# Optimization experiments

Measured on AMD Instinct MI355X. Metric: run time of the kernel, lower is better.

Reference implementation:

```python
import jax, jax.numpy as jnp
import numpy as np

B, H, W, C = 8, 32, 32, 512
NUM_HEADS = 8
NUM_GROUPS = 32
EPS = 1e-5
SKIP_SCALE = 1.0
HEAD_DIM = C // NUM_HEADS


def setup_inputs() -> dict:
    key = jax.random.key(0)
    ks = jax.random.split(key, 7)
    fan_in, fan_out = C, 3 * C
    lim_qkv = np.sqrt(6.0 / (fan_in + fan_out))
    lim_out = 1e-5 * np.sqrt(6.0 / (C + C))
    return {
        "x": jax.random.normal(ks[0], (B, H, W, C), jnp.float32),
        "norm_scale": jnp.ones((C,), jnp.float32),
        "norm_bias": jnp.zeros((C,), jnp.float32),
        "qkv_kernel": jax.random.uniform(ks[1], (C, NUM_HEADS, 3 * HEAD_DIM), jnp.float32, -lim_qkv, lim_qkv),
        "qkv_bias": jnp.zeros((NUM_HEADS, 3 * HEAD_DIM), jnp.float32),
        "out_kernel": jax.random.uniform(ks[2], (NUM_HEADS, HEAD_DIM, C), jnp.float32, -lim_out, lim_out),
        "out_bias": jnp.zeros((C,), jnp.float32),
    }


def group_norm(x, scale, bias):
    # x: (B, S, C); normalize per-group over (S, C//G), flax GroupNorm semantics
    b, s, c = x.shape
    g = NUM_GROUPS
    xg = x.reshape(b, s, g, c // g)
    mean = jnp.mean(xg, axis=(1, 3), keepdims=True)
    var = jnp.var(xg, axis=(1, 3), keepdims=True)
    xg = (xg - mean) * jax.lax.rsqrt(var + EPS)
    return xg.reshape(b, s, c) * scale + bias


def reference(x, norm_scale, norm_bias, qkv_kernel, qkv_bias, out_kernel, out_bias):
    batch_dims = x.shape[:-3]
    h, w, c = x.shape[-3:]
    xi = x.reshape(-1, h * w, c)  # (B, S, C)
    out = group_norm(xi, norm_scale, norm_bias)
    # QKV projection: (B,S,C) x (C, NH, 3*HD) -> (B,S,NH,3*HD)
    qkv = jnp.einsum('bsc,chd->bshd', out, qkv_kernel) + qkv_bias
    q, k, v = jnp.split(qkv, 3, axis=-1)  # each (B,S,NH,HD)
    scale = 1.0 / jnp.sqrt(jnp.sqrt(jnp.asarray(HEAD_DIM, jnp.float32)))
    q = q * scale
    k = k * scale
    attn = jnp.einsum('bqhd,bkhd->bhqk', q, k)
    attn = jax.nn.softmax(attn, axis=-1)
    o = jnp.einsum('bhqk,bkhd->bqhd', attn, v)
    o = jnp.einsum('bqhd,hdc->bqc', o, out_kernel) + out_bias
    o = (o + xi) * SKIP_SCALE
    return o.reshape((*batch_dims, h, w, c))
```

## Files before the change

kernel.cpp:

```cpp
#include <hip/hip_runtime.h>
#include <stdint.h>

typedef __attribute__((ext_vector_type(8))) short short8;
typedef __attribute__((ext_vector_type(4))) float f32x4;
typedef __attribute__((ext_vector_type(16))) float f32x16;
typedef __attribute__((ext_vector_type(4))) unsigned int u32x4;
typedef unsigned short u16;
typedef unsigned int u32;

#define NBATCH 8
#define SLEN 1024
#define CDIM 512
#define NHEADS 8
#define HDIM 64
#define MROWS (NBATCH*SLEN)
#define NQKV (NHEADS*3*HDIM)
#define QK_SCALE 0.35355339059327373f

__device__ inline u16 f2bf(float f){
  union{float f; uint32_t i;} v; v.f=f;
  uint32_t r = v.i + 0x7fffu + ((v.i>>16)&1u);
  return (u16)(r>>16);
}

__device__ inline u32 pk2(float a, float b){
  u32 r;
  asm("v_cvt_pk_bf16_f32 %0, %1, %2" : "=v"(r) : "v"(a), "v"(b));
  return r;
}

__device__ __forceinline__ void gld16(const u16* g, u16* l){
  __builtin_amdgcn_global_load_lds(
    (const __attribute__((address_space(1))) void*)g,
    (__attribute__((address_space(3))) void*)l, 16, 0, 0);
}

template<int N>
__global__ __launch_bounds__(256) void prep_w(const float* __restrict__ w, u16* __restrict__ wt){
  int tk = blockIdx.x / (N/64), tn = blockIdx.x % (N/64);
  int k0 = tk*64, n0 = tn*64;
  int t = threadIdx.x;
  __shared__ u16 lt[64][72];
  int row = t >> 2, slot = t & 3;
  const float* src = w + (size_t)(k0+row)*N + n0 + slot*16;
  #pragma unroll
  for (int j=0;j<16;++j)
    lt[row][slot*16+j] = f2bf(src[j]);
  __syncthreads();
  u16 tmp[16];
  #pragma unroll
  for (int j=0;j<16;++j) tmp[j] = lt[slot*16+j][row];
  *(u32x4*)(wt + (size_t)(n0+row)*512 + k0 + slot*16)     = *(u32x4*)tmp;
  *(u32x4*)(wt + (size_t)(n0+row)*512 + k0 + slot*16 + 8) = *(u32x4*)(tmp+8);
}

__global__ __launch_bounds__(256) void gn_stats(const float* __restrict__ x, float* __restrict__ stats){
  int bid = blockIdx.x;
  int b = bid >> 5, g = bid & 31;
  int t = threadIdx.x;
  const float* base = x + (size_t)b*SLEN*CDIM + g*16;
  float s1=0.f, s2=0.f;
  for (int s = t; s < SLEN; s += 256){
    const float4* p = (const float4*)(base + (size_t)s*CDIM);
    #pragma unroll
    for (int j=0;j<4;++j){
      float4 v = p[j];
      s1 += v.x+v.y+v.z+v.w;
      s2 += v.x*v.x + v.y*v.y + v.z*v.z + v.w*v.w;
    }
  }
  #pragma unroll
  for (int m=1;m<64;m<<=1){ s1 += __shfl_xor(s1,m); s2 += __shfl_xor(s2,m); }
  __shared__ float red[8];
  int wid = t>>6;
  if ((t&63)==0){ red[wid*2]=s1; red[wid*2+1]=s2; }
  __syncthreads();
  if (t==0){
    float a=0,c=0;
    #pragma unroll
    for (int w2=0;w2<4;++w2){ a+=red[w2*2]; c+=red[w2*2+1]; }
    float mean = a*(1.f/16384.f);
    float var  = c*(1.f/16384.f) - mean*mean;
    stats[bid*2]   = mean;
    stats[bid*2+1] = rsqrtf(var + 1e-5f);
  }
}

__global__ __launch_bounds__(256) void norm_cast(const float* __restrict__ x, const float* __restrict__ stats,
                        const float* __restrict__ scale, const float* __restrict__ bias,
                        u16* __restrict__ xn){
  int idx = blockIdx.x*256 + threadIdx.x;
  int m = idx >> 5, g = idx & 31;
  int b = m >> 10;
  float mean = stats[(b*32+g)*2];
  float rstd = stats[(b*32+g)*2+1];
  const float* xp = x + (size_t)m*CDIM + g*16;
  const float* sp = scale + g*16;
  const float* bp = bias + g*16;
  short8 o0, o1;
  #pragma unroll
  for (int j=0;j<16;++j){
    float v = (xp[j]-mean)*rstd*sp[j] + bp[j];
    if (j<8) o0[j] = (short)f2bf(v); else o1[j-8] = (short)f2bf(v);
  }
  short8* dst = (short8*)(xn + (size_t)m*CDIM + g*16);
  dst[0]=o0; dst[1]=o1;
}

#define BM 128
#define BN 128
#define BK 64

template<int EPI, int NT>
__global__ __launch_bounds__(256, 3) void gemm_bf16(
    const u16* __restrict__ A, const u16* __restrict__ Bt,
    const float* __restrict__ bias, const float* __restrict__ resid,
    float* __restrict__ outF,
    u16* __restrict__ qb, u16* __restrict__ kb, u16* __restrict__ vtb)
{
  const int K = CDIM;
  int t = threadIdx.x;
  int l = t & 63, wid = t >> 6;
  int g = l >> 4, c = l & 15;
  int wr = wid >> 1, wc = wid & 1;
  int nwg = gridDim.x;
  int cpx = nwg >> 3;
  int orig = blockIdx.x;
  int swz = (orig & 7)*cpx + (orig >> 3);
  int m0 = (swz / NT) * BM, n0 = (swz % NT) * BN;

  __shared__ __attribute__((aligned(16))) u16 ls[16384];
  char* lsAc = (char*)ls; char* lsBc = (char*)(ls + 8192);

  f32x4 acc[4][4];
  #pragma unroll
  for (int i=0;i<4;++i)
    #pragma unroll
    for(int j=0;j<4;++j) acc[i][j] = (f32x4)0.f;

  int lrow = l >> 3, slot = l & 7;
  int scol = ((slot ^ lrow) << 3);
  const int KT = K / BK;
  for (int kt=0; kt<KT; ++kt){
    __syncthreads();
    int kbo = kt*BK;
    #pragma unroll
    for (int q2=0; q2<4; ++q2){
      int row = wid*32 + q2*8 + lrow;
      gld16(A  + (size_t)(m0+row)*K + kbo + scol, ls        + (wid*4+q2)*512);
      gld16(Bt + (size_t)(n0+row)*K + kbo + scol, ls + 8192 + (wid*4+q2)*512);
    }
    asm volatile("s_waitcnt vmcnt(0)" ::: "memory");
    __syncthreads();
    #pragma unroll
    for (int kk=0; kk<2; ++kk){
      short8 af[4], bfr[4];
      #pragma unroll
      for (int i=0;i<4;++i){
        int rowA = wr*64 + i*16 + c;
        af[i]  = *(const short8*)(lsAc + rowA*128 + ((kk*4+g) ^ (rowA&7))*16);
        int rowB = wc*64 + i*16 + c;
        bfr[i] = *(const short8*)(lsBc + rowB*128 + ((kk*4+g) ^ (rowB&7))*16);
      }
      #pragma unroll
      for (int i=0;i<4;++i)
        #pragma unroll
        for (int j=0;j<4;++j)
          acc[i][j] = __builtin_amdgcn_mfma_f32_16x16x32_bf16(af[i], bfr[j], acc[i][j], 0,0,0);
    }
  }

  if (EPI == 0){
    int b = m0 >> 10, s0 = m0 & (SLEN-1);
    __syncthreads();
    u16* lsC = ls;
    #pragma unroll
    for (int i=0;i<4;++i){
      int rl0 = wr*64 + i*16 + g*4;
      #pragma unroll
      for (int j=0;j<4;++j){
        int cl = wc*64 + j*16 + c;
        int gcol = n0 + cl;
        int jj = gcol % 192;
        float sc_ = (jj < 128) ? QK_SCALE : 1.0f;
        float bv = bias[gcol];
        #pragma unroll
        for (int r=0;r<4;++r)
          lsC[(rl0+r)*128 + cl] = f2bf((acc[i][j][r] + bv)*sc_);
      }
    }
    __syncthreads();
    #pragma unroll
    for (int cc=0; cc<8; ++cc){
      int ch = cc*256 + t;
      int rl = ch >> 4, slot2 = ch & 15;
      int cl = slot2*8;
      int gcol = n0 + cl;
      int h = gcol / 192, jj = gcol % 192;
      int s = s0 + rl;
      u32x4 vv = *(const u32x4*)(lsC + rl*128 + cl);
      size_t rowb = ((size_t)(b*NHEADS+h))*SLEN + s;
      if (jj < 64)       __builtin_nontemporal_store(vv, (u32x4*)(qb + rowb*HDIM + jj));
      else if (jj < 128) __builtin_nontemporal_store(vv, (u32x4*)(kb + rowb*HDIM + (jj-64)));
    }
    int blk3 = (n0 >> 7) % 3;
    if (blk3 != 0){
      __syncthreads();
      u16* lsV = ls;
      #pragma unroll
      for (int i=0;i<4;++i){
        int rl0 = wr*64 + i*16 + g*4;
        #pragma unroll
        for (int j=0;j<4;++j){
          int cl = wc*64 + j*16 + c;
          int jj = (n0 + cl) % 192;
          if (jj >= 128){
            #pragma unroll
            for (int r=0;r<4;++r)
              lsV[(jj-128)*136 + rl0 + r] = f2bf(acc[i][j][r] + bias[n0+cl]);
          }
        }
      }
      __syncthreads();
      int hv = (n0 + ((blk3==1)?0:64)) / 192;
      size_t vbase = ((size_t)(b*NHEADS+hv))*HDIM*SLEN;
      #pragma unroll
      for (int cc=0; cc<4; ++cc){
        int chunk = cc*256 + t;
        int d = chunk >> 4, so = (chunk & 15)*8;
        u32x4 vv = *(const u32x4*)(lsV + d*136 + so);
        __builtin_nontemporal_store(vv, (u32x4*)(vtb + vbase + (size_t)d*SLEN + s0 + so));
      }
    }
  } else {
    #pragma unroll
    for (int i=0;i<4;++i){
      int grow = m0 + wr*64 + i*16 + g*4;
      #pragma unroll
      for (int j=0;j<4;++j){
        int gcol = n0 + wc*64 + j*16 + c;
        float bv = bias[gcol];
        #pragma unroll
        for (int r=0;r<4;++r){
          size_t off = (size_t)(grow+r)*CDIM + gcol;
          float rv = __builtin_nontemporal_load(&resid[off]);
          __builtin_nontemporal_store(acc[i][j][r] + bv + rv, &outF[off]);
        }
      }
    }
  }
}

#define PV_KS(PT, QOFF, KS) { \
    u32 A0 = pk2(PT[QOFF+0], PT[QOFF+1]); \
    u32 A1 = pk2(PT[QOFF+2], PT[QOFF+3]); \
    u32 B0 = pk2(PT[QOFF+4], PT[QOFF+5]); \
    u32 B1 = pk2(PT[QOFF+6], PT[QOFF+7]); \
    u32 A0s = __shfl_xor(A0,32), A1s = __shfl_xor(A1,32); \
    u32 B0s = __shfl_xor(B0,32), B1s = __shfl_xor(B1,32); \
    uint4 w; \
    w.x = hi ? B0s : A0;  w.y = hi ? B1s : A1; \
    w.z = hi ? B0  : A0s; w.w = hi ? B1  : A1s; \
    short8 fP; __builtin_memcpy(&fP, &w, 16); \
    o0 = __builtin_amdgcn_mfma_f32_32x32x16_bf16(fV0[KS], fP, o0, 0,0,0); \
    o1 = __builtin_amdgcn_mfma_f32_32x32x16_bf16(fV1[KS], fP, o1, 0,0,0); }

__global__ __launch_bounds__(256, 2) void attn_fused(const u16* __restrict__ qg,
  const u16* __restrict__ kg, const u16* __restrict__ vtg, u16* __restrict__ og)
{
  int bid = blockIdx.x;
  int nid = (bid & 7)*64 + (bid >> 3);
  int bh = nid >> 3, qi = nid & 7;
  int t = threadIdx.x, l = t & 63, wid = t >> 6;
  int q = l & 31, hi = l >> 5;
  int q0 = qi*128 + wid*32;

  __shared__ __attribute__((aligned(16))) u16 kl[4][4096];
  __shared__ __attribute__((aligned(16))) u16 vl[4][4096];

  const u16* qrow = qg + ((size_t)bh*SLEN + q0 + q)*HDIM + hi*8;
  short8 fQ[4];
  #pragma unroll
  for (int ds=0; ds<4; ++ds) fQ[ds] = *(const short8*)(qrow + ds*16);

  f32x16 o0, o1;
  #pragma unroll
  for (int r=0;r<16;++r){ o0[r]=0.f; o1[r]=0.f; }
  float mr = -1e30f, lsum = 0.f;

  const u16* kt_base = kg  + (size_t)bh*SLEN*HDIM;
  const u16* vt_base = vtg + (size_t)bh*HDIM*SLEN;
  int srow = l >> 3, sslot = l & 7;
  int scol8 = ((sslot ^ srow) << 3);

#define STAGE(BUF, KV) { \
    _Pragma("unroll") \
    for (int j=0;j<2;++j){ \
      int row = wid*16 + j*8 + srow; \
      int chunk = wid*2 + j; \
      gld16(kt_base + (size_t)((KV)*64 + row)*HDIM + scol8, &kl[BUF][chunk*512]); \
      gld16(vt_base + (size_t)row*SLEN + (KV)*64 + scol8,   &vl[BUF][chunk*512]); \
    } }

  STAGE(0, 0)
  STAGE(1, 1)

  int sl_q = q & 7;
  for (int kv=0; kv<16; ++kv){
    int cur = kv & 3;
    if (kv < 14) STAGE((kv+2)&3, kv+2)
    if (kv < 14)      asm volatile("s_waitcnt vmcnt(8)" ::: "memory");
    else if (kv==14)  asm volatile("s_waitcnt vmcnt(4)" ::: "memory");
    else              asm volatile("s_waitcnt vmcnt(0)" ::: "memory");
    __syncthreads();
    const u16* kb_ = &kl[cur][0];
    const u16* vb_ = &vl[cur][0];
    short8 fK0[4], fK1[4];
    #pragma unroll
    for (int ds=0; ds<4; ++ds){
      int sl = ((ds*2+hi) ^ sl_q) << 3;
      fK0[ds] = *(const short8*)(kb_ + q*64 + sl);
      fK1[ds] = *(const short8*)(kb_ + (q+32)*64 + sl);
    }
    f32x16 p0, p1;
    #pragma unroll
    for (int r=0;r<16;++r){ p0[r]=0.f; p1[r]=0.f; }
    __builtin_amdgcn_s_setprio(1);
    #pragma unroll
    for (int ds=0; ds<4; ++ds){
      p0 = __builtin_amdgcn_mfma_f32_32x32x16_bf16(fK0[ds], fQ[ds], p0, 0,0,0);
      p1 = __builtin_amdgcn_mfma_f32_32x32x16_bf16(fK1[ds], fQ[ds], p1, 0,0,0);
    }
    __builtin_amdgcn_s_setprio(0);
    float a8[8];
    #pragma unroll
    for (int r=0;r<8;++r)
      a8[r] = fmaxf(fmaxf(p0[r],p0[r+8]), fmaxf(p1[r],p1[r+8]));
    #pragma unroll
    for (int s=4;s>0;s>>=1)
      #pragma unroll
      for (int r=0;r<4;++r) if (r<s) a8[r] = fmaxf(a8[r], a8[r+s]);
    float tmax = fmaxf(a8[0], __shfl_xor(a8[0], 32));
    if (!__all(tmax <= mr + 8.0f)){
      float mn = fmaxf(mr, tmax);
      float alpha = __expf(mr - mn);
      mr = mn;
      lsum *= alpha;
      #pragma unroll
      for (int r=0;r<16;++r){ o0[r]*=alpha; o1[r]*=alpha; }
    }
    #pragma unroll
    for (int r=0;r<16;++r){ p0[r] = __expf(p0[r]-mr); p1[r] = __expf(p1[r]-mr); }
    short8 fV0[4], fV1[4];
    #pragma unroll
    for (int ks=0; ks<4; ++ks){
      int sl = ((ks*2+hi) ^ sl_q) << 3;
      fV0[ks] = *(const short8*)(vb_ + q*64 + sl);
      fV1[ks] = *(const short8*)(vb_ + (q+32)*64 + sl);
    }
    float s8[8];
    #pragma unroll
    for (int r=0;r<8;++r) s8[r] = (p0[r]+p0[r+8]) + (p1[r]+p1[r+8]);
    #pragma unroll
    for (int s=4;s>0;s>>=1)
      #pragma unroll
      for (int r=0;r<4;++r) if (r<s) s8[r] += s8[r+s];
    float rs = s8[0] + __shfl_xor(s8[0], 32);
    lsum += rs;
    __builtin_amdgcn_s_setprio(1);
    PV_KS(p0, 0, 0)
    PV_KS(p0, 8, 1)
    PV_KS(p1, 0, 2)
    PV_KS(p1, 8, 3)
    __builtin_amdgcn_s_setprio(0);
  }

  float inv = 1.f / lsum;
  int b = bh >> 3, h = bh & 7;
  u16* obase = og + ((size_t)b*SLEN + q0 + q)*CDIM + h*HDIM;
  #pragma unroll
  for (int pr=0; pr<8; ++pr){
    int d = ((2*pr)&3) + 8*(pr>>1) + 4*hi;
    *(u32*)(obase + d)      = pk2(o0[2*pr]*inv, o0[2*pr+1]*inv);
    *(u32*)(obase + 32 + d) = pk2(o1[2*pr]*inv, o1[2*pr+1]*inv);
  }
}

extern "C" void kernel_launch(void* const* d_in, const int* in_sizes, int n_in,
                              void* d_out, int out_size, void* d_ws, size_t ws_size,
                              hipStream_t stream){
  const float* x      = (const float*)d_in[0];
  const float* nscale = (const float*)d_in[1];
  const float* nbias  = (const float*)d_in[2];
  const float* wqkv   = (const float*)d_in[3];
  const float* bqkv   = (const float*)d_in[4];
  const float* wout   = (const float*)d_in[5];
  const float* bout   = (const float*)d_in[6];
  float* out = (float*)d_out;

  char* ws = (char*)d_ws;
  size_t off = 0;
  auto alloc = [&](size_t bytes){ void* p = ws + off; off += (bytes + 255) & ~255ull; return p; };
  float* stats  = (float*)alloc(256*2*sizeof(float));
  u16* wqkv_t = (u16*)alloc((size_t)NQKV*CDIM*2);
  u16* wout_t = (u16*)alloc((size_t)CDIM*CDIM*2);
  u16* xn     = (u16*)alloc((size_t)MROWS*CDIM*2);
  u16* qb     = (u16*)alloc((size_t)MROWS*CDIM*2);
  u16* kb     = (u16*)alloc((size_t)MROWS*CDIM*2);
  u16* vtb    = (u16*)alloc((size_t)MROWS*CDIM*2);
  u16* ob     = (u16*)alloc((size_t)MROWS*CDIM*2);

  prep_w<NQKV><<<dim3(8*(NQKV/64)), dim3(256), 0, stream>>>(wqkv, wqkv_t);
  prep_w<CDIM><<<dim3(8*(CDIM/64)), dim3(256), 0, stream>>>(wout, wout_t);
  gn_stats <<<dim3(256), dim3(256), 0, stream>>>(x, stats);
  norm_cast<<<dim3((MROWS*32)/256), dim3(256), 0, stream>>>(x, stats, nscale, nbias, xn);
  gemm_bf16<0,12><<<dim3(768), dim3(256), 0, stream>>>(xn, wqkv_t, bqkv, nullptr, nullptr, qb, kb, vtb);
  attn_fused<<<dim3(512), dim3(256), 0, stream>>>(qb, kb, vtb, ob);
  gemm_bf16<1,4><<<dim3(256), dim3(256), 0, stream>>>(ob, wout_t, bout, x, out, nullptr, nullptr, nullptr);
}
```

Before: 101.0 us.

## Process two KV tiles per iteration in attention and use permlane32 swaps

After: 95.19 us. -5.7%, faster.

```diff
diff --git a/kernel.cpp b/kernel.cpp
--- a/kernel.cpp
+++ b/kernel.cpp
@@ -251,19 +251,18 @@
   }
 }
 
-#define PV_KS(PT, QOFF, KS) { \
+#define PV_KS(PT, QOFF, V0, V1, KS) { \
     u32 A0 = pk2(PT[QOFF+0], PT[QOFF+1]); \
     u32 A1 = pk2(PT[QOFF+2], PT[QOFF+3]); \
     u32 B0 = pk2(PT[QOFF+4], PT[QOFF+5]); \
     u32 B1 = pk2(PT[QOFF+6], PT[QOFF+7]); \
-    u32 A0s = __shfl_xor(A0,32), A1s = __shfl_xor(A1,32); \
-    u32 B0s = __shfl_xor(B0,32), B1s = __shfl_xor(B1,32); \
+    auto r0_ = __builtin_amdgcn_permlane32_swap((int)A0, (int)B0, false, false); \
+    auto r1_ = __builtin_amdgcn_permlane32_swap((int)A1, (int)B1, false, false); \
     uint4 w; \
-    w.x = hi ? B0s : A0;  w.y = hi ? B1s : A1; \
-    w.z = hi ? B0  : A0s; w.w = hi ? B1  : A1s; \
+    w.x = (u32)r0_[0]; w.y = (u32)r1_[0]; w.z = (u32)r0_[1]; w.w = (u32)r1_[1]; \
     short8 fP; __builtin_memcpy(&fP, &w, 16); \
-    o0 = __builtin_amdgcn_mfma_f32_32x32x16_bf16(fV0[KS], fP, o0, 0,0,0); \
-    o1 = __builtin_amdgcn_mfma_f32_32x32x16_bf16(fV1[KS], fP, o1, 0,0,0); }
+    o0 = __builtin_amdgcn_mfma_f32_32x32x16_bf16(V0[KS], fP, o0, 0,0,0); \
+    o1 = __builtin_amdgcn_mfma_f32_32x32x16_bf16(V1[KS], fP, o1, 0,0,0); }
 
 __global__ __launch_bounds__(256, 2) void attn_fused(const u16* __restrict__ qg,
   const u16* __restrict__ kg, const u16* __restrict__ vtg, u16* __restrict__ og)
@@ -304,43 +303,62 @@
 
   STAGE(0, 0)
   STAGE(1, 1)
+  STAGE(2, 2)
+  STAGE(3, 3)
 
   int sl_q = q & 7;
-  for (int kv=0; kv<16; ++kv){
-    int cur = kv & 3;
-    if (kv < 14) STAGE((kv+2)&3, kv+2)
-    if (kv < 14)      asm volatile("s_waitcnt vmcnt(8)" ::: "memory");
-    else if (kv==14)  asm volatile("s_waitcnt vmcnt(4)" ::: "memory");
-    else              asm volatile("s_waitcnt vmcnt(0)" ::: "memory");
-    __syncthreads();
-    const u16* kb_ = &kl[cur][0];
-    const u16* vb_ = &vl[cur][0];
-    short8 fK0[4], fK1[4];
+  for (int p=0; p<8; ++p){
+    if (p < 7) asm volatile("s_waitcnt vmcnt(8)" ::: "memory");
+    else       asm volatile("s_waitcnt vmcnt(0)" ::: "memory");
+    __syncthreads();
+    int tA = 2*p, tB = 2*p+1;
+    const u16* kA = &kl[tA&3][0]; const u16* kB = &kl[tB&3][0];
+    const u16* vA = &vl[tA&3][0]; const u16* vB = &vl[tB&3][0];
+    short8 fKA0[4], fKA1[4], fKB0[4], fKB1[4];
     #pragma unroll
     for (int ds=0; ds<4; ++ds){
       int sl = ((ds*2+hi) ^ sl_q) << 3;
-      fK0[ds] = *(const short8*)(kb_ + q*64 + sl);
-      fK1[ds] = *(const short8*)(kb_ + (q+32)*64 + sl);
-    }
-    f32x16 p0, p1;
-    #pragma unroll
-    for (int r=0;r<16;++r){ p0[r]=0.f; p1[r]=0.f; }
+      fKA0[ds] = *(const short8*)(kA + q*64 + sl);
+      fKA1[ds] = *(const short8*)(kA + (q+32)*64 + sl);
+      fKB0[ds] = *(const short8*)(kB + q*64 + sl);
+      fKB1[ds] = *(const short8*)(kB + (q+32)*64 + sl);
+    }
+    f32x16 pA0, pA1, pB0, pB1;
+    #pragma unroll
+    for (int r=0;r<16;++r){ pA0[r]=0.f; pA1[r]=0.f; pB0[r]=0.f; pB1[r]=0.f; }
     __builtin_amdgcn_s_setprio(1);
     #pragma unroll
     for (int ds=0; ds<4; ++ds){
-      p0 = __builtin_amdgcn_mfma_f32_32x32x16_bf16(fK0[ds], fQ[ds], p0, 0,0,0);
-      p1 = __builtin_amdgcn_mfma_f32_32x32x16_bf16(fK1[ds], fQ[ds], p1, 0,0,0);
+      pA0 = __builtin_amdgcn_mfma_f32_32x32x16_bf16(fKA0[ds], fQ[ds], pA0, 0,0,0);
+      pB0 = __builtin_amdgcn_mfma_f32_32x32x16_bf16(fKB0[ds], fQ[ds], pB0, 0,0,0);
+      pA1 = __builtin_amdgcn_mfma_f32_32x32x16_bf16(fKA1[ds], fQ[ds], pA1, 0,0,0);
+      pB1 = __builtin_amdgcn_mfma_f32_32x32x16_bf16(fKB1[ds], fQ[ds], pB1, 0,0,0);
     }
     __builtin_amdgcn_s_setprio(0);
+    short8 fVA0[4], fVA1[4], fVB0[4], fVB1[4];
+    #pragma unroll
+    for (int ks=0; ks<4; ++ks){
+      int sl = ((ks*2+hi) ^ sl_q) << 3;
+      fVA0[ks] = *(const short8*)(vA + q*64 + sl);
+      fVA1[ks] = *(const short8*)(vA + (q+32)*64 + sl);
+      fVB0[ks] = *(const short8*)(vB + q*64 + sl);
+      fVB1[ks] = *(const short8*)(vB + (q+32)*64 + sl);
+    }
     float a8[8];
     #pragma unroll
-    for (int r=0;r<8;++r)
-      a8[r] = fmaxf(fmaxf(p0[r],p0[r+8]), fmaxf(p1[r],p1[r+8]));
+    for (int r=0;r<8;++r){
+      float ma = fmaxf(fmaxf(pA0[r],pA0[r+8]), fmaxf(pA1[r],pA1[r+8]));
+      float mb = fmaxf(fmaxf(pB0[r],pB0[r+8]), fmaxf(pB1[r],pB1[r+8]));
+      a8[r] = fmaxf(ma, mb);
+    }
     #pragma unroll
     for (int s=4;s>0;s>>=1)
       #pragma unroll
       for (int r=0;r<4;++r) if (r<s) a8[r] = fmaxf(a8[r], a8[r+s]);
-    float tmax = fmaxf(a8[0], __shfl_xor(a8[0], 32));
+    auto rm_ = __builtin_amdgcn_permlane32_swap(
+        __builtin_bit_cast(int, a8[0]), __builtin_bit_cast(int, a8[0]), false, false);
+    float tmax = fmaxf(a8[0], fmaxf(__builtin_bit_cast(float, rm_[0]),
+                                    __builtin_bit_cast(float, rm_[1])));
     if (!__all(tmax <= mr + 8.0f)){
       float mn = fmaxf(mr, tmax);
       float alpha = __expf(mr - mn);
@@ -350,29 +368,37 @@
       for (int r=0;r<16;++r){ o0[r]*=alpha; o1[r]*=alpha; }
     }
     #pragma unroll
-    for (int r=0;r<16;++r){ p0[r] = __expf(p0[r]-mr); p1[r] = __expf(p1[r]-mr); }
-    short8 fV0[4], fV1[4];
-    #pragma unroll
-    for (int ks=0; ks<4; ++ks){
-      int sl = ((ks*2+hi) ^ sl_q) << 3;
-      fV0[ks] = *(const short8*)(vb_ + q*64 + sl);
-      fV1[ks] = *(const short8*)(vb_ + (q+32)*64 + sl);
+    for (int r=0;r<16;++r){
+      pA0[r] = __expf(pA0[r]-mr); pA1[r] = __expf(pA1[r]-mr);
+      pB0[r] = __expf(pB0[r]-mr); pB1[r] = __expf(pB1[r]-mr);
     }
     float s8[8];
     #pragma unroll
-    for (int r=0;r<8;++r) s8[r] = (p0[r]+p0[r+8]) + (p1[r]+p1[r+8]);
+    for (int r=0;r<8;++r)
+      s8[r] = ((pA0[r]+pA0[r+8]) + (pA1[r]+pA1[r+8]))
+            + ((pB0[r]+pB0[r+8]) + (pB1[r]+pB1[r+8]));
     #pragma unroll
     for (int s=4;s>0;s>>=1)
       #pragma unroll
       for (int r=0;r<4;++r) if (r<s) s8[r] += s8[r+s];
-    float rs = s8[0] + __shfl_xor(s8[0], 32);
-    lsum += rs;
+    auto rs_ = __builtin_amdgcn_permlane32_swap(
+        __builtin_bit_cast(int, s8[0]), __builtin_bit_cast(int, s8[0]), false, false);
+    lsum += __builtin_bit_cast(float, rs_[0]) + __builtin_bit_cast(float, rs_[1]);
     __builtin_amdgcn_s_setprio(1);
-    PV_KS(p0, 0, 0)
-    PV_KS(p0, 8, 1)
-    PV_KS(p1, 0, 2)
-    PV_KS(p1, 8, 3)
+    PV_KS(pA0, 0, fVA0, fVA1, 0)
+    PV_KS(pA0, 8, fVA0, fVA1, 1)
+    PV_KS(pA1, 0, fVA0, fVA1, 2)
+    PV_KS(pA1, 8, fVA0, fVA1, 3)
+    PV_KS(pB0, 0, fVB0, fVB1, 0)
+    PV_KS(pB0, 8, fVB0, fVB1, 1)
+    PV_KS(pB1, 0, fVB0, fVB1, 2)
+    PV_KS(pB1, 8, fVB0, fVB1, 3)
     __builtin_amdgcn_s_setprio(0);
+    __syncthreads();
+    if (p < 6){
+      STAGE((2*p+4)&3, 2*p+4)
+      STAGE((2*p+5)&3, 2*p+5)
+    }
   }
 
   float inv = 1.f / lsum;
```
